# Performance work log

Measured on AMD Instinct MI355X. Metric: run time of the kernel, lower is better.

The kernel has to match this reference:

```python
import jax, jax.numpy as jnp
import numpy as np
import math

EMBED = 256
HEADS = 8
HD = EMBED // HEADS  # 32
NB = 3               # n_behaviors
C = NB * NB + 1      # 10 behavior-pair classes
NUM_BUCKETS = 32
MAX_DIST = 40
EPS = 1e-12
B, L = 4, 512


def _rel_bucket(seq_len, num_buckets=NUM_BUCKETS, max_distance=MAX_DIST):
    """T5-style relative position buckets, matching RelativePositionBias._relative_position_bucket."""
    pos = jnp.arange(seq_len)
    relative_position = pos[None, :] - pos[:, None]  # k - q
    n = -relative_position
    nb = num_buckets // 2
    ret = (n < 0).astype(jnp.int32) * nb
    n = jnp.abs(n)
    max_exact = nb // 2
    is_small = n < max_exact
    nf = jnp.maximum(n, 1).astype(jnp.float32)  # clamp to avoid log(0); masked by is_small anyway
    val_large = max_exact + (jnp.log(nf / max_exact) / math.log(max_distance / max_exact) * (nb - max_exact)).astype(jnp.int32)
    val_large = jnp.minimum(val_large, nb - 1)
    return ret + jnp.where(is_small, n, val_large)


def setup_inputs() -> dict:
    key = jax.random.key(0)
    ks = jax.random.split(key, 12)
    s = 0.02
    return {
        "input_tensor": jax.random.normal(ks[0], (B, L, EMBED), jnp.float32),
        "attention_mask": jnp.zeros((B, 1, L, L), jnp.float32),
        "type_seq": jax.random.randint(ks[1], (B, L), 0, NB + 1),
        "Wq": jax.random.normal(ks[2], (NB + 1, EMBED, HEADS, HD), jnp.float32) * s,
        "Wk": jax.random.normal(ks[3], (NB + 1, EMBED, HEADS, HD), jnp.float32) * s,
        "Wv": jax.random.normal(ks[4], (NB + 1, EMBED, HEADS, HD), jnp.float32) * s,
        "W1": jax.random.normal(ks[5], (NB, HEADS, HD, HD), jnp.float32) * s,
        "alpha1": jax.random.normal(ks[6], (C, NB, HEADS), jnp.float32),
        "W2": jax.random.normal(ks[7], (NB, HEADS, HD, HD), jnp.float32) * s,
        "alpha2": jax.random.normal(ks[8], (C, NB, HEADS), jnp.float32),
        "rp_tables": jax.random.normal(ks[9], (C, NUM_BUCKETS, HEADS), jnp.float32) * s,
        "ln_gamma": jnp.ones((EMBED,), jnp.float32),
        "ln_beta": jnp.zeros((EMBED,), jnp.float32),
    }


def reference(input_tensor, attention_mask, type_seq, Wq, Wk, Wv, W1, alpha1, W2, alpha2, rp_tables, ln_gamma, ln_beta):
    bsz, seq_len, emb = input_tensor.shape
    ts = type_seq
    # behavior pair matrix: 0 if either side is padding, else (tq-1)*NB + tk in [1, NB^2]
    bm = ((ts[:, :, None] * ts[:, None, :]) != 0).astype(jnp.int32)
    bm = bm * ((ts[:, :, None] - 1) * NB + ts[:, None, :])  # [B,L,L]

    # --- relative position bias, gathered per behavior pair ---
    bucket = _rel_bucket(seq_len)                 # [L,L]
    vals = rp_tables[:, bucket, :]                # [C,L,L,H]
    qi = jnp.arange(seq_len)[None, :, None]
    ki = jnp.arange(seq_len)[None, None, :]
    bias = vals[bm, qi, ki]                       # [B,L,L,H] gathered along C per pair
    bias = jnp.transpose(bias, (0, 3, 1, 2))      # [B,H,L,L]

    # --- behavior-gated QKV ---
    oh = jax.nn.one_hot(ts, NB + 1, dtype=input_tensor.dtype)  # [B,L,NB+1]
    q = jnp.einsum('BLH,bHhd,BLb->BhLd', input_tensor, Wq, oh)
    k = jnp.einsum('BLH,bHhd,BLb->BhLd', input_tensor, Wk, oh)
    v = jnp.einsum('BLH,bHhd,BLb->BhLd', input_tensor, Wv, oh)

    # --- bilinear scores with per-pair mixing matrices ---
    W1_ = jnp.einsum('bhmn,Cbh->Chmn', W1, jax.nn.softmax(alpha1, axis=1))
    att_all = jnp.einsum('BhQm,Chmn,BhKn->BhQKC', q, W1_, k)  # [B,H,L,L,C]
    scores = jnp.take_along_axis(att_all, bm[:, None, :, :, None], axis=4)[..., 0]
    scores = scores * (1.0 / math.sqrt(HD)) + bias + attention_mask
    probs = jax.nn.softmax(scores, axis=-1)  # dropout=0.0 -> identity

    # --- behavior-mixed value aggregation ---
    W2_ = jnp.einsum('bhmn,Cbh->Chmn', W2, jax.nn.softmax(alpha2, axis=1))
    oh_bm = jax.nn.one_hot(bm, C, dtype=probs.dtype)          # [B,L,L,C]
    pC = probs[:, :, :, :, None] * oh_bm[:, None]             # [B,H,L,L,C]
    ctx = jnp.einsum('BhQKC,Chnm,BhKn->BhQm', pC, W2_, v)     # [B,H,L,d]

    ctx = jnp.transpose(ctx, (0, 2, 1, 3)).reshape(bsz, seq_len, emb)
    x = ctx + input_tensor  # out_dropout=0.0
    mu = jnp.mean(x, axis=-1, keepdims=True)
    var = jnp.mean(jnp.square(x - mu), axis=-1, keepdims=True)
    return (x - mu) / jnp.sqrt(var + EPS) * ln_gamma + ln_beta
```

## Files before the change

kernel.cpp:

```cpp
#include <hip/hip_runtime.h>
#include <math.h>

#define BB 4
#define LL 512
#define EMB 256
#define NH 8
#define HD 32
#define NB_ 3
#define CCN 10
#define NBKT 32
#define SCALE 0.17677669529663687f

typedef __bf16 bf16_t;
typedef __attribute__((ext_vector_type(8))) bf16_t bf16x8;
typedef __attribute__((ext_vector_type(4))) float f32x4;

__device__ __forceinline__ unsigned short f2b(float f) {
    unsigned int u = __float_as_uint(f);
    u += 0x7FFF + ((u >> 16) & 1);
    return (unsigned short)(u >> 16);
}
__device__ __forceinline__ float b2f(unsigned short s) {
    return __uint_as_float(((unsigned int)s) << 16);
}
__device__ __forceinline__ unsigned pack2(float a, float b) {
    return (unsigned)f2b(a) | ((unsigned)f2b(b) << 16);
}
__device__ __forceinline__ int bm_of(int tq, int tk) {
    return (tq * tk != 0) ? ((tq - 1) * 3 + tk) : 0;
}
__device__ __forceinline__ unsigned long long shfl_up64(unsigned long long v, int d) {
    unsigned lo = (unsigned)__shfl_up((int)(unsigned)v, d, 64);
    unsigned hi = (unsigned)__shfl_up((int)(v >> 32), d, 64);
    return (((unsigned long long)hi) << 32) | lo;
}

__device__ __forceinline__ void sort512(const int* __restrict__ tsb, int* spk,
                                        unsigned long long* wtll, int* msc, int tid) {
    int ty0 = tsb[2 * tid], ty1 = tsb[2 * tid + 1];
    unsigned long long pk = (1ULL << (16 * ty0)) + (1ULL << (16 * ty1));
    unsigned long long v = pk;
    int lane = tid & 63;
#pragma unroll
    for (int off = 1; off < 64; off <<= 1) {
        unsigned long long o = shfl_up64(v, off);
        if (lane >= off) v += o;
    }
    int w = tid >> 6;
    if (lane == 63) wtll[w] = v;
    __syncthreads();
    unsigned long long pre = 0, tot = 0;
#pragma unroll
    for (int i = 0; i < 4; i++) {
        unsigned long long xx = wtll[i];
        if (i < w) pre += xx;
        tot += xx;
    }
    v += pre;
    unsigned long long excl = v - pk;
    int c0 = (int)(tot & 0xFFFF), c1 = (int)((tot >> 16) & 0xFFFF);
    int c2 = (int)((tot >> 32) & 0xFFFF), c3 = (int)((tot >> 48) & 0xFFFF);
    int ub0 = 0, ub1 = c0, ub2 = c0 + c1, ub3 = c0 + c1 + c2;
    if (tid == 0) {
        int pc0 = (c0 + 31) & ~31, pc1 = (c1 + 31) & ~31, pc2 = (c2 + 31) & ~31, pc3 = (c3 + 31) & ~31;
        int pb1 = pc0, pb2 = pc0 + pc1, pb3 = pc0 + pc1 + pc2;
        msc[0] = 0;  msc[1] = pb1; msc[2] = pb2; msc[3] = pb3;
        msc[4] = ub0; msc[5] = ub1; msc[6] = ub2; msc[7] = ub3;
        msc[8] = c0; msc[9] = c1; msc[10] = c2; msc[11] = c3;
        msc[12] = (pb3 + pc3 + 63) & ~63;
    }
    int bases[4] = {ub0, ub1, ub2, ub3};
    int r0 = (int)((excl >> (16 * ty0)) & 0xFFFF);
    unsigned long long excl1 = excl + (1ULL << (16 * ty0));
    int r1 = (int)((excl1 >> (16 * ty1)) & 0xFFFF);
    spk[bases[ty0] + r0] = (ty0 << 16) | (2 * tid);
    spk[bases[ty1] + r1] = (ty1 << 16) | (2 * tid + 1);
    __syncthreads();
}

__device__ __forceinline__ void pad_lookup(const int* msc, int pos, int& real, int& upos, int& seg) {
    seg = (pos >= msc[1]) + (pos >= msc[2]) + (pos >= msc[3]);
    int r = pos - msc[seg];
    real = (r < msc[8 + seg]) ? 1 : 0;
    upos = msc[4 + seg] + r;
}

__global__ void k_pre(const float* __restrict__ A1, const float* __restrict__ W1,
                      const float* __restrict__ A2, const float* __restrict__ W2,
                      const float* __restrict__ Wq, const float* __restrict__ Wk, const float* __restrict__ Wv,
                      const float* __restrict__ am, const int* __restrict__ ts,
                      float* __restrict__ W1s, float* __restrict__ W2s,
                      unsigned short* __restrict__ W1Tb, unsigned short* __restrict__ W2Tb,
                      unsigned short* __restrict__ Wt, int* __restrict__ mflagArr,
                      int* __restrict__ spkg, int* __restrict__ mscg, int* __restrict__ kpadg,
                      short* __restrict__ tblg) {
    __shared__ float cmb[32 * 33];
    __shared__ unsigned short ls[64 * 264];
    __shared__ int reds[4];
    __shared__ int spk_s[LL];
    __shared__ unsigned long long wtll[4];
    __shared__ int msc_s[16];
    int g = blockIdx.x, tid = threadIdx.x;
    if (g < 160) {
        int idx = g;
        const float* alpha = (idx < 80) ? A1 : A2;
        const float* W     = (idx < 80) ? W1 : W2;
        float* Ws          = (idx < 80) ? W1s : W2s;
        unsigned short* WT = (idx < 80) ? W1Tb : W2Tb;
        idx %= 80;
        int cc = idx / NH, h = idx % NH;
        float a0 = alpha[cc * NB_ * NH + 0 * NH + h];
        float a1 = alpha[cc * NB_ * NH + 1 * NH + h];
        float a2 = alpha[cc * NB_ * NH + 2 * NH + h];
        float mx = fmaxf(a0, fmaxf(a1, a2));
        float e0 = __expf(a0 - mx), e1 = __expf(a1 - mx), e2 = __expf(a2 - mx);
        float inv = 1.0f / (e0 + e1 + e2);
        e0 *= inv; e1 *= inv; e2 *= inv;
        for (int i = tid; i < HD * HD; i += 256) {
            int m = i >> 5, n = i & 31;
            float acc = e0 * W[((0 * NH + h) * HD + m) * HD + n]
                      + e1 * W[((1 * NH + h) * HD + m) * HD + n]
                      + e2 * W[((2 * NH + h) * HD + m) * HD + n];
            cmb[m * 33 + n] = acc;
        }
        __syncthreads();
        for (int i = tid; i < HD * HD; i += 256) {
            int a = i >> 5, bq = i & 31;
            Ws[((cc * NH + h) * HD + a) * HD + bq] = cmb[a * 33 + bq];
            WT[((size_t)(cc * NH + h) * HD + a) * HD + bq] = f2b(cmb[bq * 33 + a]);
        }
        return;
    }
    if (g < 208) {
        int t = g - 160;
        int tw = t >> 2, ob = t & 3;
        int which = tw >> 2, ty = tw & 3;
        const float* src = ((which == 0) ? Wq : (which == 1) ? Wk : Wv) + (size_t)ty * EMB * EMB;
        int out0 = ob * 64;
        for (int it = 0; it < 16; it++) {
            int e = it * 16 + (tid >> 4);
            int o4 = (tid & 15) * 4;
            float4 v = *(const float4*)&src[(size_t)e * EMB + out0 + o4];
            ls[(o4 + 0) * 264 + e] = f2b(v.x);
            ls[(o4 + 1) * 264 + e] = f2b(v.y);
            ls[(o4 + 2) * 264 + e] = f2b(v.z);
            ls[(o4 + 3) * 264 + e] = f2b(v.w);
        }
        __syncthreads();
        int out = tid >> 2, ech = (tid & 3) * 8;
        unsigned short* dst = Wt + (size_t)tw * EMB * EMB + (size_t)(out0 + out) * EMB;
        const unsigned short* srcl = &ls[out * 264];
#pragma unroll
        for (int jj = 0; jj < 8; jj++)
            *(uint4*)&dst[ech + jj * 32] = *(const uint4*)&srcl[ech + jj * 32];
        return;
    }
    if (g < 464) {
        int idx = g - 208;
        const uint4* p = (const uint4*)am + (size_t)idx * 1024;
        unsigned o = 0;
#pragma unroll
        for (int j = 0; j < 4; j++) {
            uint4 v = p[tid + j * 256];
            o |= v.x | v.y | v.z | v.w;
        }
        int wv = __any(o != 0);
        if ((tid & 63) == 0) reds[tid >> 6] = wv;
        __syncthreads();
        if (tid == 0) mflagArr[idx] = reds[0] | reds[1] | reds[2] | reds[3];
        return;
    }
    if (g < 468) {
        int b = g - 464;
        sort512(ts + b * LL, spk_s, wtll, msc_s, tid);
        for (int i = tid; i < LL; i += 256) spkg[b * LL + i] = spk_s[i];
        if (tid < 16) mscg[b * 16 + tid] = msc_s[tid];
        int KT = msc_s[12];
        for (int pos = tid; pos < KT; pos += 256) {
            int real, upos, seg;
            pad_lookup(msc_s, pos, real, upos, seg);
            int orig = real ? (spk_s[upos] & 0xFFFF) : 0x3FF;
            kpadg[b * 640 + pos] = (seg << 20) | ((real ? upos : 0) << 10) | orig;
        }
        return;
    }
    for (int d = tid; d < LL; d += 256) {
        int v;
        if (d < 8) v = d;
        else {
            double r = log((double)d / 8.0) / log(5.0);
            v = 8 + (int)(r * 8.0);
            if (v > 15) v = 15;
        }
        tblg[d] = (short)v;
    }
}

__global__ __launch_bounds__(256, 4) void k_qkv(
    const float* __restrict__ x, const int* __restrict__ spkg, const int* __restrict__ mscg,
    const unsigned short* __restrict__ Wt,
    unsigned short* __restrict__ qp, unsigned short* __restrict__ kp,
    unsigned short* __restrict__ vpT) {
    __shared__ int spk[LL];
    __shared__ int msc[16];
    __shared__ unsigned short vt_l[128 * 33];

    int g = blockIdx.x, tid = threadIdx.x;
    int ns = g % 6, gb = g / 6;
    int b = gb >> 4, tb = gb & 15, i0 = tb * 32;
    int which = ns >> 1, nh = ns & 1;
    int wave = tid >> 6, lane = tid & 63, quad = lane >> 4, col = lane & 15;

    spk[tid] = spkg[b * LL + tid];
    spk[tid + 256] = spkg[b * LL + tid + 256];
    if (tid < 16) msc[tid] = mscg[b * 16 + tid];
    __syncthreads();

    bf16x8 afr[2][8];
#pragma unroll
    for (int mt = 0; mt < 2; mt++) {
        int orig = spk[i0 + mt * 16 + col] & 0xFFFF;
        const float* xr = &x[(size_t)(b * LL + orig) * EMB];
#pragma unroll
        for (int kc = 0; kc < 8; kc++) {
            float4 v0 = *(const float4*)&xr[kc * 32 + quad * 8];
            float4 v1 = *(const float4*)&xr[kc * 32 + quad * 8 + 4];
            uint4 up;
            up.x = pack2(v0.x, v0.y); up.y = pack2(v0.z, v0.w);
            up.z = pack2(v1.x, v1.y); up.w = pack2(v1.z, v1.w);
            afr[mt][kc] = *(bf16x8*)&up;
        }
    }
    int t_start = spk[i0] >> 16, t_end = spk[i0 + 31] >> 16;
    unsigned short* outp = (which == 0) ? qp : kp;

    for (int ty = t_start; ty <= t_end; ty++) {
        f32x4 acc[2][2];
#pragma unroll
        for (int mt = 0; mt < 2; mt++)
#pragma unroll
            for (int nt = 0; nt < 2; nt++) acc[mt][nt] = (f32x4){0.f, 0.f, 0.f, 0.f};
        const unsigned short* wsrc = Wt + (size_t)(which * 4 + ty) * EMB * EMB + (size_t)(nh * 128) * EMB;
        const unsigned short* w0 = &wsrc[(size_t)((wave * 2 + 0) * 16 + col) * EMB + quad * 8];
        const unsigned short* w1 = &wsrc[(size_t)((wave * 2 + 1) * 16 + col) * EMB + quad * 8];
#pragma unroll
        for (int kc = 0; kc < 8; kc++) {
            bf16x8 b0 = *(const bf16x8*)&w0[kc * 32];
            bf16x8 b1 = *(const bf16x8*)&w1[kc * 32];
            acc[0][0] = __builtin_amdgcn_mfma_f32_16x16x32_bf16(afr[0][kc], b0, acc[0][0], 0, 0, 0);
            acc[0][1] = __builtin_amdgcn_mfma_f32_16x16x32_bf16(afr[0][kc], b1, acc[0][1], 0, 0, 0);
            acc[1][0] = __builtin_amdgcn_mfma_f32_16x16x32_bf16(afr[1][kc], b0, acc[1][0], 0, 0, 0);
            acc[1][1] = __builtin_amdgcn_mfma_f32_16x16x32_bf16(afr[1][kc], b1, acc[1][1], 0, 0, 0);
        }
        if (which < 2) {
#pragma unroll
            for (int mt = 0; mt < 2; mt++)
#pragma unroll
                for (int r = 0; r < 4; r++) {
                    int tokloc = mt * 16 + quad * 4 + r;
                    int tty = spk[i0 + tokloc] >> 16;
                    if (tty != ty) continue;
#pragma unroll
                    for (int nt = 0; nt < 2; nt++) {
                        int n = nh * 128 + (wave * 2 + nt) * 16 + col;
                        int h = n >> 5, d = n & 31;
                        outp[((size_t)(b * NH + h) * LL + i0 + tokloc) * HD + d] = f2b(acc[mt][nt][r]);
                    }
                }
        } else {
#pragma unroll
            for (int mt = 0; mt < 2; mt++)
#pragma unroll
                for (int nt = 0; nt < 2; nt++) {
                    int ln = (wave * 2 + nt) * 16 + col;
#pragma unroll
                    for (int r = 0; r < 4; r++)
                        vt_l[ln * 33 + mt * 16 + quad * 4 + r] = f2b(acc[mt][nt][r]);
                }
            __syncthreads();
            int ub = msc[4 + ty], cnt = msc[8 + ty], pb = msc[ty];
            int lo = ub - i0; if (lo < 0) lo = 0;
            int hi = ub + cnt - i0; if (hi > 32) hi = 32;
            int run = hi - lo;
            int pbase = pb + i0 + lo - ub;
            int rowbase = b * 256 + nh * 128;
            int t32 = tid & 31;
            if (t32 < run) {
                for (int rr = tid >> 5; rr < 128; rr += 8)
                    vpT[(size_t)(rowbase + rr) * 640 + pbase + t32] = vt_l[rr * 33 + lo + t32];
            }
            __syncthreads();
        }
    }
}

#define SCP 648
#define OFF_UN   20736
#define OFF_QTB  29184
#define OFF_KPAD 33536
#define OFF_TBL  36096
#define OFF_RPL  37120
#define OFF_QOR  38400
#define OFF_QTY  38464
#define OFF_INV  38528
#define SM_TOTAL 38592
__global__ __launch_bounds__(256, 4) void k_attn(
    const unsigned short* __restrict__ qp, const unsigned short* __restrict__ kp,
    const unsigned short* __restrict__ vpT,
    const int* __restrict__ spkg, const int* __restrict__ mscg, const int* __restrict__ kpadg,
    const short* __restrict__ tblg,
    const float* __restrict__ rp, const float* __restrict__ am,
    const float* __restrict__ W1s, const float* __restrict__ W2s,
    const unsigned short* __restrict__ W1Tb, const unsigned short* __restrict__ W2Tb,
    const int* __restrict__ mflagArr, float* __restrict__ ctx) {
    __shared__ __align__(16) char smem[SM_TOTAL];
    __shared__ int msk_s;
    unsigned short* scu = (unsigned short*)smem;
    unsigned short* qstb = (unsigned short*)(smem + OFF_UN);
    float* sb   = (float*)(smem + OFF_UN);
    unsigned short* qtb = (unsigned short*)(smem + OFF_QTB);
    unsigned short* sbb = (unsigned short*)(smem + OFF_QTB);
    int*   kpad = (int*)(smem + OFF_KPAD);
    short* tbl  = (short*)(smem + OFF_TBL);
    float* rp_l = (float*)(smem + OFF_RPL);
    int*   qor_l = (int*)(smem + OFF_QOR);
    int*   qty_l = (int*)(smem + OFF_QTY);
    float* inv_l = (float*)(smem + OFF_INV);

    int blk = blockIdx.x;
    int b = blk >> 8, h = (blk >> 5) & 7, q16 = blk & 31;
    int i0q = q16 * 16;
    int tid = threadIdx.x;
    int wave = tid >> 6, lane = tid & 63, quad = lane >> 4, col = lane & 15;
    int bh = b * NH + h;

    int KT = mscg[b * 16 + 12];
    if (wave == 0) {
        int v = 0;
#pragma unroll
        for (int j = 0; j < 4; j++) v |= mflagArr[lane + 64 * j];
        int anyv = __any(v != 0);
        if (lane == 0) msk_s = anyv;
    }
    if (tid < 16) {
        int v = spkg[b * LL + i0q + tid];
        qor_l[tid] = v & 0xFFFF; qty_l[tid] = v >> 16;
    }
    for (int pos = tid; pos < KT; pos += 256) kpad[pos] = kpadg[b * 640 + pos];
    ((int*)tbl)[tid] = ((const int*)tblg)[tid];
    for (int i = tid; i < CCN * NBKT; i += 256) rp_l[i] = rp[i * NH + h];
    {
        int q = tid >> 4, m2 = (tid & 15) * 2;
        ((unsigned*)qstb)[q * 20 + (tid & 15)] =
            *(const unsigned*)&qp[((size_t)bh * LL + i0q + q) * HD + m2];
    }
    __syncthreads();

    int qor_r[4], qty_r[4];
#pragma unroll
    for (int r = 0; r < 4; r++) { qor_r[r] = qor_l[quad * 4 + r]; qty_r[r] = qty_l[quad * 4 + r]; }
    bool uniq = (qty_l[0] == qty_l[15]);
    int tqu = qty_l[0];
    int tA = qty_l[0], tB = qty_l[15];
    bool two = false;
    if (!uniq) {
        two = true;
#pragma unroll
        for (int i = 0; i < 16; i++) {
            int t = qty_l[i];
            two = two && (t == tA || t == tB);
        }
    }
    int mz = (msk_s == 0);

    if (uniq) {
#pragma unroll
        for (int it = 0; it < 2; it++) {
            int t8 = wave * 2 + it;
            int tk = t8 >> 1, nhf = t8 & 1;
            int bmv = bm_of(tqu, tk);
            bf16x8 a = *(const bf16x8*)&qstb[col * 40 + quad * 8];
            bf16x8 bb = *(const bf16x8*)&W1Tb[((size_t)(bmv * NH + h) * HD + nhf * 16 + col) * HD + quad * 8];
            f32x4 d = {0.f, 0.f, 0.f, 0.f};
            d = __builtin_amdgcn_mfma_f32_16x16x32_bf16(a, bb, d, 0, 0, 0);
#pragma unroll
            for (int r = 0; r < 4; r++)
                qtb[(quad * 4 + r) * 136 + tk * 32 + nhf * 16 + col] = f2b(d[r]);
        }
    } else if (two) {
#pragma unroll
        for (int it = 0; it < 2; it++) {
            int t8 = wave * 2 + it;
            int tk = t8 >> 1, nhf = t8 & 1;
            bf16x8 a = *(const bf16x8*)&qstb[col * 40 + quad * 8];
            bf16x8 bA = *(const bf16x8*)&W1Tb[((size_t)(bm_of(tA, tk) * NH + h) * HD + nhf * 16 + col) * HD + quad * 8];
            bf16x8 bBv = *(const bf16x8*)&W1Tb[((size_t)(bm_of(tB, tk) * NH + h) * HD + nhf * 16 + col) * HD + quad * 8];
            f32x4 dA = {0.f, 0.f, 0.f, 0.f};
            f32x4 dB = {0.f, 0.f, 0.f, 0.f};
            dA = __builtin_amdgcn_mfma_f32_16x16x32_bf16(a, bA, dA, 0, 0, 0);
            dB = __builtin_amdgcn_mfma_f32_16x16x32_bf16(a, bBv, dB, 0, 0, 0);
#pragma unroll
            for (int r = 0; r < 4; r++) {
                float val = (qty_r[r] == tA) ? dA[r] : dB[r];
                qtb[(quad * 4 + r) * 136 + tk * 32 + nhf * 16 + col] = f2b(val);
            }
        }
    } else {
        for (int i = tid; i < 16 * 128; i += 256) {
            int q = i >> 7, r = i & 127, tk = r >> 5, n = r & 31;
            int bmv = bm_of(qty_l[q], tk);
            const float* wb = &W1s[((bmv * NH + h) * HD) * HD + n];
            float acc = 0.f;
#pragma unroll
            for (int m = 0; m < HD; m++) acc += b2f(qstb[q * 40 + m]) * wb[m * HD];
            qtb[q * 136 + tk * 32 + n] = f2b(acc);
        }
    }
    __syncthreads();

    const float* amb = am + (size_t)b * LL * LL;
    int ntiles = KT >> 4;
    for (int tile = wave; tile < ntiles; tile += 4) {
        int kb = tile * 16;
        int kv0 = kpad[kb];
        if ((kv0 & 0x3FF) == 0x3FF) {
#pragma unroll
            for (int r = 0; r < 4; r++) scu[(quad * 4 + r) * SCP + kb + col] = 0xFF80;
            continue;
        }
        int tkt = kv0 >> 20;
        int kpi = kb + col;
        int kv = kpad[kpi];
        int ko = kv & 0x3FF;
        int upos = (kv >> 10) & 0x3FF;
        bool real = (ko != 0x3FF);
        bf16x8 bfr;
        if (real) bfr = *(const bf16x8*)&kp[((size_t)bh * LL + upos) * HD + quad * 8];
        else { uint4 z = make_uint4(0, 0, 0, 0); bfr = *(bf16x8*)&z; }
        bf16x8 a = *(const bf16x8*)&qtb[col * 136 + tkt * 32 + quad * 8];
        f32x4 d = {0.f, 0.f, 0.f, 0.f};
        d = __builtin_amdgcn_mfma_f32_16x16x32_bf16(a, bfr, d, 0, 0, 0);
        if (!real) {
#pragma unroll
            for (int r = 0; r < 4; r++) scu[(quad * 4 + r) * SCP + kpi] = 0xFF80;
        } else {
#pragma unroll
            for (int r = 0; r < 4; r++) {
                int q = quad * 4 + r;
                int qo = qor_r[r];
                int dd = qo - ko;
                int ad = dd < 0 ? -dd : dd;
                int bk = (dd < 0 ? 16 : 0) + (int)tbl[ad];
                float sv = d[r] * SCALE + rp_l[bm_of(qty_r[r], tkt) * NBKT + bk];
                if (!mz) sv += amb[(size_t)qo * LL + ko];
                scu[q * SCP + kpi] = f2b(sv);
            }
        }
    }
    __syncthreads();

    {
        int gq = tid >> 4, t16 = tid & 15;
        float mx = -1e30f;
        for (int kk = t16; kk < KT; kk += 16) mx = fmaxf(mx, b2f(scu[gq * SCP + kk]));
#pragma unroll
        for (int off = 1; off < 16; off <<= 1) mx = fmaxf(mx, __shfl_xor(mx, off, 16));
        float sum = 0.f;
        for (int kk = t16; kk < KT; kk += 16) {
            int idx = gq * SCP + kk;
            float e = __expf(b2f(scu[idx]) - mx);
            scu[idx] = f2b(e); sum += e;
        }
#pragma unroll
        for (int off = 1; off < 16; off <<= 1) sum += __shfl_xor(sum, off, 16);
        if (t16 == 0) inv_l[gq] = 1.0f / sum;
    }
    __syncthreads();

    const unsigned short* vbase = &vpT[(size_t)(b * 256 + h * 32) * 640];
    f32x4 accv[2];
    accv[0] = (f32x4){0.f, 0.f, 0.f, 0.f};
    accv[1] = (f32x4){0.f, 0.f, 0.f, 0.f};
    {
        int pb = mscg[b * 16 + wave];
        int cnt = mscg[b * 16 + 8 + wave];
        int g0 = pb >> 5, g1 = (pb + cnt + 31) >> 5;
        for (int gg = g0; gg < g1; ++gg) {
            int loc = gg << 5;
            bf16x8 a = *(const bf16x8*)&scu[col * SCP + loc + quad * 8];
            bf16x8 b0 = *(const bf16x8*)&vbase[(size_t)col * 640 + loc + quad * 8];
            bf16x8 b1 = *(const bf16x8*)&vbase[(size_t)(col + 16) * 640 + loc + quad * 8];
            accv[0] = __builtin_amdgcn_mfma_f32_16x16x32_bf16(a, b0, accv[0], 0, 0, 0);
            accv[1] = __builtin_amdgcn_mfma_f32_16x16x32_bf16(a, b1, accv[1], 0, 0, 0);
        }
    }
#pragma unroll
    for (int hh = 0; hh < 2; hh++)
#pragma unroll
        for (int r = 0; r < 4; r++) {
            int q = quad * 4 + r, n = col + 16 * hh;
            float fin = accv[hh][r];
            sb[q * 132 + wave * 32 + n] = fin;
            sbb[q * 136 + wave * 32 + n] = f2b(fin);
        }
    __syncthreads();

    if (uniq) {
        if (wave < 2) {
            int mhf = wave;
            f32x4 d = {0.f, 0.f, 0.f, 0.f};
#pragma unroll
            for (int tk = 0; tk < 4; tk++) {
                int bmv = bm_of(tqu, tk);
                bf16x8 a = *(const bf16x8*)&sbb[col * 136 + tk * 32 + quad * 8];
                bf16x8 bb = *(const bf16x8*)&W2Tb[((size_t)(bmv * NH + h) * HD + mhf * 16 + col) * HD + quad * 8];
                d = __builtin_amdgcn_mfma_f32_16x16x32_bf16(a, bb, d, 0, 0, 0);
            }
#pragma unroll
            for (int r = 0; r < 4; r++) {
                int q = quad * 4 + r;
                ctx[((size_t)(b * LL + qor_l[q])) * EMB + h * HD + mhf * 16 + col] = d[r] * inv_l[q];
            }
        }
    } else if (two) {
        int myT = (wave < 2) ? tA : tB;
        int mhf = wave & 1;
        f32x4 d = {0.f, 0.f, 0.f, 0.f};
#pragma unroll
        for (int tk = 0; tk < 4; tk++) {
            int bmv = bm_of(myT, tk);
            bf16x8 a = *(const bf16x8*)&sbb[col * 136 + tk * 32 + quad * 8];
            bf16x8 bb = *(const bf16x8*)&W2Tb[((size_t)(bmv * NH + h) * HD + mhf * 16 + col) * HD + quad * 8];
            d = __builtin_amdgcn_mfma_f32_16x16x32_bf16(a, bb, d, 0, 0, 0);
        }
#pragma unroll
        for (int r = 0; r < 4; r++) {
            int q = quad * 4 + r;
            if (qty_l[q] == myT)
                ctx[((size_t)(b * LL + qor_l[q])) * EMB + h * HD + mhf * 16 + col] = d[r] * inv_l[q];
        }
    } else {
        int m = tid & 31, qq = tid >> 5;
#pragma unroll
        for (int rep = 0; rep < 2; rep++) {
            int qi = qq + 8 * rep;
            int tq = qty_l[qi];
            float acc = 0.f;
#pragma unroll
            for (int tk2 = 0; tk2 < 4; tk2++) {
                int bmv = bm_of(tq, tk2);
                const float* wb = &W2s[((bmv * NH + h) * HD) * HD + m];
                const float* sbp = &sb[qi * 132 + tk2 * 32];
                for (int n = 0; n < HD; n++) acc += sbp[n] * wb[n * HD];
            }
            int qo = qor_l[qi];
            ctx[((size_t)(b * LL + qo)) * EMB + h * HD + m] = acc * inv_l[qi];
        }
    }
}

__global__ void k_ln(const float* __restrict__ ctx, const float* __restrict__ x,
                     const float* __restrict__ gamma, const float* __restrict__ beta,
                     float* __restrict__ out) {
    int wave = threadIdx.x >> 6, lane = threadIdx.x & 63;
    int tok = blockIdx.x * 4 + wave;
    size_t base = (size_t)tok * EMB + lane * 4;
    float4 c = *(const float4*)&ctx[base];
    float4 xi = *(const float4*)&x[base];
    float4 v;
    v.x = c.x + xi.x; v.y = c.y + xi.y; v.z = c.z + xi.z; v.w = c.w + xi.w;
    float s = v.x + v.y + v.z + v.w;
    float s2 = v.x * v.x + v.y * v.y + v.z * v.z + v.w * v.w;
#pragma unroll
    for (int off = 1; off < 64; off <<= 1) {
        s += __shfl_xor(s, off, 64);
        s2 += __shfl_xor(s2, off, 64);
    }
    float mu = s * (1.0f / EMB);
    float var = s2 * (1.0f / EMB) - mu * mu;
    float r = rsqrtf(var + 1e-12f);
    float4 gg = *(const float4*)&gamma[lane * 4];
    float4 bb = *(const float4*)&beta[lane * 4];
    float4 o;
    o.x = (v.x - mu) * r * gg.x + bb.x;
    o.y = (v.y - mu) * r * gg.y + bb.y;
    o.z = (v.z - mu) * r * gg.z + bb.z;
    o.w = (v.w - mu) * r * gg.w + bb.w;
    *(float4*)&out[base] = o;
}

extern "C" void kernel_launch(void* const* d_in, const int* in_sizes, int n_in,
                              void* d_out, int out_size, void* d_ws, size_t ws_size,
                              hipStream_t stream) {
    const float* x  = (const float*)d_in[0];
    const float* am = (const float*)d_in[1];
    const int*   ts = (const int*)d_in[2];
    const float* Wq = (const float*)d_in[3];
    const float* Wk = (const float*)d_in[4];
    const float* Wv = (const float*)d_in[5];
    const float* W1 = (const float*)d_in[6];
    const float* a1 = (const float*)d_in[7];
    const float* W2 = (const float*)d_in[8];
    const float* a2 = (const float*)d_in[9];
    const float* rp = (const float*)d_in[10];
    const float* g  = (const float*)d_in[11];
    const float* be = (const float*)d_in[12];
    float* out = (float*)d_out;

    float* ws  = (float*)d_ws;
    float* W1s = ws;
    float* W2s = ws + 81920;
    unsigned short* W1Tb = (unsigned short*)(ws + 163840);
    unsigned short* W2Tb = (unsigned short*)(ws + 204800);
    int* mflagArr = (int*)(ws + 245760);
    int* spkg = (int*)(ws + 246016);
    int* mscg = (int*)(ws + 248064);
    int* kpadg = (int*)(ws + 248128);
    short* tblg = (short*)(ws + 250688);
    unsigned short* qp = (unsigned short*)(ws + 250944);
    unsigned short* kp = qp + BB * NH * LL * HD;
    unsigned short* vpT = kp + BB * NH * LL * HD;
    float* ctx = (float*)(vpT + BB * 256 * 640);
    unsigned short* Wt = (unsigned short*)ctx;

    hipLaunchKernelGGL(k_pre, dim3(469), dim3(256), 0, stream,
                       a1, W1, a2, W2, Wq, Wk, Wv, am, ts, W1s, W2s, W1Tb, W2Tb, Wt,
                       mflagArr, spkg, mscg, kpadg, tblg);
    hipLaunchKernelGGL(k_qkv, dim3(384), dim3(256), 0, stream, x, spkg, mscg, Wt, qp, kp, vpT);
    hipLaunchKernelGGL(k_attn, dim3(BB * NH * 32), dim3(256), 0, stream,
                       qp, kp, vpT, spkg, mscg, kpadg, tblg, rp, am, W1s, W2s, W1Tb, W2Tb, mflagArr, ctx);
    hipLaunchKernelGGL(k_ln, dim3(BB * LL / 4), dim3(256), 0, stream, ctx, x, g, be, out);
}
```

Baseline: 127.5 us.

## Fuse LayerNorm into attention via completion counters and rebalance prep work across kernels

The W1/W2 mixing precompute and the attention-mask nonzero scan move from the prep kernel into extra blocks of the QKV kernel, so the prep kernel shrinks to 53 blocks and those jobs run alongside the projection. The separate LayerNorm kernel is removed. The last of the 8 head blocks for each query tile, found with an atomic counter, applies residual-add plus LayerNorm to that tile's rows. The mask flag becomes a single atomicOr word, and the kpad copy is vectorised. This removes one launch and the round trip of the ctx tensor, but adds a threadfence and atomic per block and depends on counters being reset in the prep kernel every call.

```diff
diff --git a/kernel.cpp b/kernel.cpp
--- a/kernel.cpp
+++ b/kernel.cpp
@@ -85,54 +85,17 @@
     upos = msc[4 + seg] + r;
 }
 
-__global__ void k_pre(const float* __restrict__ A1, const float* __restrict__ W1,
-                      const float* __restrict__ A2, const float* __restrict__ W2,
-                      const float* __restrict__ Wq, const float* __restrict__ Wk, const float* __restrict__ Wv,
-                      const float* __restrict__ am, const int* __restrict__ ts,
-                      float* __restrict__ W1s, float* __restrict__ W2s,
-                      unsigned short* __restrict__ W1Tb, unsigned short* __restrict__ W2Tb,
-                      unsigned short* __restrict__ Wt, int* __restrict__ mflagArr,
+__global__ void k_pre(const float* __restrict__ Wq, const float* __restrict__ Wk, const float* __restrict__ Wv,
+                      const int* __restrict__ ts, unsigned short* __restrict__ Wt,
                       int* __restrict__ spkg, int* __restrict__ mscg, int* __restrict__ kpadg,
-                      short* __restrict__ tblg) {
-    __shared__ float cmb[32 * 33];
+                      short* __restrict__ tblg, int* __restrict__ cntg) {
     __shared__ unsigned short ls[64 * 264];
-    __shared__ int reds[4];
     __shared__ int spk_s[LL];
     __shared__ unsigned long long wtll[4];
     __shared__ int msc_s[16];
     int g = blockIdx.x, tid = threadIdx.x;
-    if (g < 160) {
-        int idx = g;
-        const float* alpha = (idx < 80) ? A1 : A2;
-        const float* W     = (idx < 80) ? W1 : W2;
-        float* Ws          = (idx < 80) ? W1s : W2s;
-        unsigned short* WT = (idx < 80) ? W1Tb : W2Tb;
-        idx %= 80;
-        int cc = idx / NH, h = idx % NH;
-        float a0 = alpha[cc * NB_ * NH + 0 * NH + h];
-        float a1 = alpha[cc * NB_ * NH + 1 * NH + h];
-        float a2 = alpha[cc * NB_ * NH + 2 * NH + h];
-        float mx = fmaxf(a0, fmaxf(a1, a2));
-        float e0 = __expf(a0 - mx), e1 = __expf(a1 - mx), e2 = __expf(a2 - mx);
-        float inv = 1.0f / (e0 + e1 + e2);
-        e0 *= inv; e1 *= inv; e2 *= inv;
-        for (int i = tid; i < HD * HD; i += 256) {
-            int m = i >> 5, n = i & 31;
-            float acc = e0 * W[((0 * NH + h) * HD + m) * HD + n]
-                      + e1 * W[((1 * NH + h) * HD + m) * HD + n]
-                      + e2 * W[((2 * NH + h) * HD + m) * HD + n];
-            cmb[m * 33 + n] = acc;
-        }
-        __syncthreads();
-        for (int i = tid; i < HD * HD; i += 256) {
-            int a = i >> 5, bq = i & 31;
-            Ws[((cc * NH + h) * HD + a) * HD + bq] = cmb[a * 33 + bq];
-            WT[((size_t)(cc * NH + h) * HD + a) * HD + bq] = f2b(cmb[bq * 33 + a]);
-        }
-        return;
-    }
-    if (g < 208) {
-        int t = g - 160;
+    if (g < 48) {
+        int t = g;
         int tw = t >> 2, ob = t & 3;
         int which = tw >> 2, ty = tw & 3;
         const float* src = ((which == 0) ? Wq : (which == 1) ? Wk : Wv) + (size_t)ty * EMB * EMB;
@@ -155,23 +118,22 @@
             *(uint4*)&dst[ech + jj * 32] = *(const uint4*)&srcl[ech + jj * 32];
         return;
     }
-    if (g < 464) {
-        int idx = g - 208;
-        const uint4* p = (const uint4*)am + (size_t)idx * 1024;
-        unsigned o = 0;
-#pragma unroll
-        for (int j = 0; j < 4; j++) {
-            uint4 v = p[tid + j * 256];
-            o |= v.x | v.y | v.z | v.w;
-        }
-        int wv = __any(o != 0);
-        if ((tid & 63) == 0) reds[tid >> 6] = wv;
-        __syncthreads();
-        if (tid == 0) mflagArr[idx] = reds[0] | reds[1] | reds[2] | reds[3];
+    if (g == 48) {
+        for (int d = tid; d < LL; d += 256) {
+            int v;
+            if (d < 8) v = d;
+            else {
+                double r = log((double)d / 8.0) / log(5.0);
+                v = 8 + (int)(r * 8.0);
+                if (v > 15) v = 15;
+            }
+            tblg[d] = (short)v;
+        }
+        if (tid < 129) cntg[tid] = 0;
         return;
     }
-    if (g < 468) {
-        int b = g - 464;
+    {
+        int b = g - 49;
         sort512(ts + b * LL, spk_s, wtll, msc_s, tid);
         for (int i = tid; i < LL; i += 256) spkg[b * LL + i] = spk_s[i];
         if (tid < 16) mscg[b * 16 + tid] = msc_s[tid];
@@ -182,30 +144,72 @@
             int orig = real ? (spk_s[upos] & 0xFFFF) : 0x3FF;
             kpadg[b * 640 + pos] = (seg << 20) | ((real ? upos : 0) << 10) | orig;
         }
-        return;
-    }
-    for (int d = tid; d < LL; d += 256) {
-        int v;
-        if (d < 8) v = d;
-        else {
-            double r = log((double)d / 8.0) / log(5.0);
-            v = 8 + (int)(r * 8.0);
-            if (v > 15) v = 15;
-        }
-        tblg[d] = (short)v;
     }
 }
 
 __global__ __launch_bounds__(256, 4) void k_qkv(
     const float* __restrict__ x, const int* __restrict__ spkg, const int* __restrict__ mscg,
     const unsigned short* __restrict__ Wt,
+    const float* __restrict__ A1, const float* __restrict__ W1,
+    const float* __restrict__ A2, const float* __restrict__ W2,
+    const float* __restrict__ am,
+    float* __restrict__ W1s, float* __restrict__ W2s,
+    unsigned short* __restrict__ W1Tb, unsigned short* __restrict__ W2Tb,
+    int* __restrict__ cntg,
     unsigned short* __restrict__ qp, unsigned short* __restrict__ kp,
     unsigned short* __restrict__ vpT) {
     __shared__ int spk[LL];
     __shared__ int msc[16];
-    __shared__ unsigned short vt_l[128 * 33];
+    __shared__ __align__(16) unsigned short vt_l[128 * 33];
 
     int g = blockIdx.x, tid = threadIdx.x;
+
+    if (g >= 384) {
+        int gg = g - 384;
+        if (gg < 160) {
+            float* cmbf = (float*)vt_l;
+            int idx = gg;
+            const float* alpha = (idx < 80) ? A1 : A2;
+            const float* W     = (idx < 80) ? W1 : W2;
+            float* Ws          = (idx < 80) ? W1s : W2s;
+            unsigned short* WT = (idx < 80) ? W1Tb : W2Tb;
+            idx %= 80;
+            int cc = idx / NH, h = idx % NH;
+            float a0 = alpha[cc * NB_ * NH + 0 * NH + h];
+            float a1 = alpha[cc * NB_ * NH + 1 * NH + h];
+            float a2 = alpha[cc * NB_ * NH + 2 * NH + h];
+            float mx = fmaxf(a0, fmaxf(a1, a2));
+            float e0 = __expf(a0 - mx), e1 = __expf(a1 - mx), e2 = __expf(a2 - mx);
+            float inv = 1.0f / (e0 + e1 + e2);
+            e0 *= inv; e1 *= inv; e2 *= inv;
+            for (int i = tid; i < HD * HD; i += 256) {
+                int m = i >> 5, n = i & 31;
+                float acc = e0 * W[((0 * NH + h) * HD + m) * HD + n]
+                          + e1 * W[((1 * NH + h) * HD + m) * HD + n]
+                          + e2 * W[((2 * NH + h) * HD + m) * HD + n];
+                cmbf[m * 33 + n] = acc;
+            }
+            __syncthreads();
+            for (int i = tid; i < HD * HD; i += 256) {
+                int a = i >> 5, bq = i & 31;
+                Ws[((cc * NH + h) * HD + a) * HD + bq] = cmbf[a * 33 + bq];
+                WT[((size_t)(cc * NH + h) * HD + a) * HD + bq] = f2b(cmbf[bq * 33 + a]);
+            }
+        } else {
+            int idx = gg - 160;
+            const uint4* p = (const uint4*)am + (size_t)idx * 1024;
+            unsigned o = 0;
+#pragma unroll
+            for (int j = 0; j < 4; j++) {
+                uint4 v = p[tid + j * 256];
+                o |= v.x | v.y | v.z | v.w;
+            }
+            int wv = __any(o != 0);
+            if ((tid & 63) == 0 && wv) atomicOr(&cntg[128], 1);
+        }
+        return;
+    }
+
     int ns = g % 6, gb = g / 6;
     int b = gb >> 4, tb = gb & 15, i0 = tb * 32;
     int which = ns >> 1, nh = ns & 1;
@@ -312,9 +316,12 @@
     const float* __restrict__ rp, const float* __restrict__ am,
     const float* __restrict__ W1s, const float* __restrict__ W2s,
     const unsigned short* __restrict__ W1Tb, const unsigned short* __restrict__ W2Tb,
-    const int* __restrict__ mflagArr, float* __restrict__ ctx) {
+    int* __restrict__ cntg, float* __restrict__ ctx,
+    const float* __restrict__ x, const float* __restrict__ gamma, const float* __restrict__ beta,
+    float* __restrict__ out) {
     __shared__ __align__(16) char smem[SM_TOTAL];
     __shared__ int msk_s;
+    __shared__ int done_s;
     unsigned short* scu = (unsigned short*)smem;
     unsigned short* qstb = (unsigned short*)(smem + OFF_UN);
     float* sb   = (float*)(smem + OFF_UN);
@@ -335,18 +342,12 @@
     int bh = b * NH + h;
 
     int KT = mscg[b * 16 + 12];
-    if (wave == 0) {
-        int v = 0;
-#pragma unroll
-        for (int j = 0; j < 4; j++) v |= mflagArr[lane + 64 * j];
-        int anyv = __any(v != 0);
-        if (lane == 0) msk_s = anyv;
-    }
+    if (tid == 0) msk_s = cntg[128];
     if (tid < 16) {
         int v = spkg[b * LL + i0q + tid];
         qor_l[tid] = v & 0xFFFF; qty_l[tid] = v >> 16;
     }
-    for (int pos = tid; pos < KT; pos += 256) kpad[pos] = kpadg[b * 640 + pos];
+    if (tid < (KT >> 2)) ((int4*)kpad)[tid] = ((const int4*)(kpadg + b * 640))[tid];
     ((int*)tbl)[tid] = ((const int*)tblg)[tid];
     for (int i = tid; i < CCN * NBKT; i += 256) rp_l[i] = rp[i * NH + h];
     {
@@ -557,36 +558,65 @@
             ctx[((size_t)(b * LL + qo)) * EMB + h * HD + m] = acc * inv_l[qi];
         }
     }
-}
-
-__global__ void k_ln(const float* __restrict__ ctx, const float* __restrict__ x,
-                     const float* __restrict__ gamma, const float* __restrict__ beta,
-                     float* __restrict__ out) {
-    int wave = threadIdx.x >> 6, lane = threadIdx.x & 63;
-    int tok = blockIdx.x * 4 + wave;
-    size_t base = (size_t)tok * EMB + lane * 4;
-    float4 c = *(const float4*)&ctx[base];
-    float4 xi = *(const float4*)&x[base];
-    float4 v;
-    v.x = c.x + xi.x; v.y = c.y + xi.y; v.z = c.z + xi.z; v.w = c.w + xi.w;
-    float s = v.x + v.y + v.z + v.w;
-    float s2 = v.x * v.x + v.y * v.y + v.z * v.z + v.w * v.w;
-#pragma unroll
-    for (int off = 1; off < 64; off <<= 1) {
-        s += __shfl_xor(s, off, 64);
-        s2 += __shfl_xor(s2, off, 64);
-    }
-    float mu = s * (1.0f / EMB);
-    float var = s2 * (1.0f / EMB) - mu * mu;
-    float r = rsqrtf(var + 1e-12f);
-    float4 gg = *(const float4*)&gamma[lane * 4];
-    float4 bb = *(const float4*)&beta[lane * 4];
-    float4 o;
-    o.x = (v.x - mu) * r * gg.x + bb.x;
-    o.y = (v.y - mu) * r * gg.y + bb.y;
-    o.z = (v.z - mu) * r * gg.z + bb.z;
-    o.w = (v.w - mu) * r * gg.w + bb.w;
-    *(float4*)&out[base] = o;
+
+    __threadfence();
+    __syncthreads();
+    if (tid == 0) done_s = atomicAdd(&cntg[b * 32 + q16], 1);
+    __syncthreads();
+    if (done_s == 7) {
+        __threadfence();
+        int qi = tid >> 4, t16 = tid & 15;
+        int tok = qor_l[qi];
+        size_t base = ((size_t)(b * LL + tok)) * EMB + t16 * 16;
+        float4 c0 = *(const float4*)&ctx[base + 0];
+        float4 c1 = *(const float4*)&ctx[base + 4];
+        float4 c2 = *(const float4*)&ctx[base + 8];
+        float4 c3 = *(const float4*)&ctx[base + 12];
+        float4 x0 = *(const float4*)&x[base + 0];
+        float4 x1 = *(const float4*)&x[base + 4];
+        float4 x2 = *(const float4*)&x[base + 8];
+        float4 x3 = *(const float4*)&x[base + 12];
+        c0.x += x0.x; c0.y += x0.y; c0.z += x0.z; c0.w += x0.w;
+        c1.x += x1.x; c1.y += x1.y; c1.z += x1.z; c1.w += x1.w;
+        c2.x += x2.x; c2.y += x2.y; c2.z += x2.z; c2.w += x2.w;
+        c3.x += x3.x; c3.y += x3.y; c3.z += x3.z; c3.w += x3.w;
+        float s = c0.x + c0.y + c0.z + c0.w + c1.x + c1.y + c1.z + c1.w
+                + c2.x + c2.y + c2.z + c2.w + c3.x + c3.y + c3.z + c3.w;
+        float s2 = c0.x*c0.x + c0.y*c0.y + c0.z*c0.z + c0.w*c0.w
+                 + c1.x*c1.x + c1.y*c1.y + c1.z*c1.z + c1.w*c1.w
+                 + c2.x*c2.x + c2.y*c2.y + c2.z*c2.z + c2.w*c2.w
+                 + c3.x*c3.x + c3.y*c3.y + c3.z*c3.z + c3.w*c3.w;
+#pragma unroll
+        for (int off = 1; off < 16; off <<= 1) {
+            s += __shfl_xor(s, off, 16);
+            s2 += __shfl_xor(s2, off, 16);
+        }
+        float mu = s * (1.0f / EMB);
+        float var = s2 * (1.0f / EMB) - mu * mu;
+        float rr = rsqrtf(var + 1e-12f);
+        int go = t16 * 16;
+        float4 g0 = *(const float4*)&gamma[go + 0];
+        float4 g1 = *(const float4*)&gamma[go + 4];
+        float4 g2 = *(const float4*)&gamma[go + 8];
+        float4 g3 = *(const float4*)&gamma[go + 12];
+        float4 b0 = *(const float4*)&beta[go + 0];
+        float4 b1 = *(const float4*)&beta[go + 4];
+        float4 b2 = *(const float4*)&beta[go + 8];
+        float4 b3 = *(const float4*)&beta[go + 12];
+        float4 o0, o1, o2, o3;
+        o0.x = (c0.x - mu) * rr * g0.x + b0.x; o0.y = (c0.y - mu) * rr * g0.y + b0.y;
+        o0.z = (c0.z - mu) * rr * g0.z + b0.z; o0.w = (c0.w - mu) * rr * g0.w + b0.w;
+        o1.x = (c1.x - mu) * rr * g1.x + b1.x; o1.y = (c1.y - mu) * rr * g1.y + b1.y;
+        o1.z = (c1.z - mu) * rr * g1.z + b1.z; o1.w = (c1.w - mu) * rr * g1.w + b1.w;
+        o2.x = (c2.x - mu) * rr * g2.x + b2.x; o2.y = (c2.y - mu) * rr * g2.y + b2.y;
+        o2.z = (c2.z - mu) * rr * g2.z + b2.z; o2.w = (c2.w - mu) * rr * g2.w + b2.w;
+        o3.x = (c3.x - mu) * rr * g3.x + b3.x; o3.y = (c3.y - mu) * rr * g3.y + b3.y;
+        o3.z = (c3.z - mu) * rr * g3.z + b3.z; o3.w = (c3.w - mu) * rr * g3.w + b3.w;
+        *(float4*)&out[base + 0] = o0;
+        *(float4*)&out[base + 4] = o1;
+        *(float4*)&out[base + 8] = o2;
+        *(float4*)&out[base + 12] = o3;
+    }
 }
 
 extern "C" void kernel_launch(void* const* d_in, const int* in_sizes, int n_in,
@@ -612,7 +642,7 @@
     float* W2s = ws + 81920;
     unsigned short* W1Tb = (unsigned short*)(ws + 163840);
     unsigned short* W2Tb = (unsigned short*)(ws + 204800);
-    int* mflagArr = (int*)(ws + 245760);
+    int* cntg = (int*)(ws + 245760);
     int* spkg = (int*)(ws + 246016);
     int* mscg = (int*)(ws + 248064);
     int* kpadg = (int*)(ws + 248128);
@@ -623,11 +653,12 @@
     float* ctx = (float*)(vpT + BB * 256 * 640);
     unsigned short* Wt = (unsigned short*)ctx;
 
-    hipLaunchKernelGGL(k_pre, dim3(469), dim3(256), 0, stream,
-                       a1, W1, a2, W2, Wq, Wk, Wv, am, ts, W1s, W2s, W1Tb, W2Tb, Wt,
-                       mflagArr, spkg, mscg, kpadg, tblg);
-    hipLaunchKernelGGL(k_qkv, dim3(384), dim3(256), 0, stream, x, spkg, mscg, Wt, qp, kp, vpT);
+    hipLaunchKernelGGL(k_pre, dim3(53), dim3(256), 0, stream,
+                       Wq, Wk, Wv, ts, Wt, spkg, mscg, kpadg, tblg, cntg);
+    hipLaunchKernelGGL(k_qkv, dim3(800), dim3(256), 0, stream,
+                       x, spkg, mscg, Wt, a1, W1, a2, W2, am, W1s, W2s, W1Tb, W2Tb, cntg,
+                       qp, kp, vpT);
     hipLaunchKernelGGL(k_attn, dim3(BB * NH * 32), dim3(256), 0, stream,
-                       qp, kp, vpT, spkg, mscg, kpadg, tblg, rp, am, W1s, W2s, W1Tb, W2Tb, mflagArr, ctx);
-    hipLaunchKernelGGL(k_ln, dim3(BB * LL / 4), dim3(256), 0, stream, ctx, x, g, be, out);
-}
+                       qp, kp, vpT, spkg, mscg, kpadg, tblg, rp, am, W1s, W2s, W1Tb, W2Tb,
+                       cntg, ctx, x, g, be, out);
+}
```

Result: slower. 252.1 us (+97.7%).

## Move W1/W2 mixing and mask scan into QKV kernel as extra blocks

Applied to the files above, without the earlier changes.

The mixing-matrix softmax/combination and the attention-mask nonzero scan move out of the pre kernel into extra blocks of the QKV projection kernel, so they run alongside the projection. The pre kernel shrinks to weight transpose, sorting and the bucket table. The per-block mask flag array becomes a single atomically-ORed flag that the pre kernel zeroes, which removes the 256-entry reduction in every attention block. The kpad staging load is vectorised to int4. The aim is to shorten the critical path of the small pre kernel. The risks are that the QKV kernel now has more blocks competing for compute units, and that the int4 copy assumes KT is a multiple of 4.

```diff
diff --git a/kernel.cpp b/kernel.cpp
--- a/kernel.cpp
+++ b/kernel.cpp
@@ -85,54 +85,17 @@
     upos = msc[4 + seg] + r;
 }
 
-__global__ void k_pre(const float* __restrict__ A1, const float* __restrict__ W1,
-                      const float* __restrict__ A2, const float* __restrict__ W2,
-                      const float* __restrict__ Wq, const float* __restrict__ Wk, const float* __restrict__ Wv,
-                      const float* __restrict__ am, const int* __restrict__ ts,
-                      float* __restrict__ W1s, float* __restrict__ W2s,
-                      unsigned short* __restrict__ W1Tb, unsigned short* __restrict__ W2Tb,
-                      unsigned short* __restrict__ Wt, int* __restrict__ mflagArr,
+__global__ void k_pre(const float* __restrict__ Wq, const float* __restrict__ Wk, const float* __restrict__ Wv,
+                      const int* __restrict__ ts, unsigned short* __restrict__ Wt,
                       int* __restrict__ spkg, int* __restrict__ mscg, int* __restrict__ kpadg,
-                      short* __restrict__ tblg) {
-    __shared__ float cmb[32 * 33];
+                      short* __restrict__ tblg, int* __restrict__ cntg) {
     __shared__ unsigned short ls[64 * 264];
-    __shared__ int reds[4];
     __shared__ int spk_s[LL];
     __shared__ unsigned long long wtll[4];
     __shared__ int msc_s[16];
     int g = blockIdx.x, tid = threadIdx.x;
-    if (g < 160) {
-        int idx = g;
-        const float* alpha = (idx < 80) ? A1 : A2;
-        const float* W     = (idx < 80) ? W1 : W2;
-        float* Ws          = (idx < 80) ? W1s : W2s;
-        unsigned short* WT = (idx < 80) ? W1Tb : W2Tb;
-        idx %= 80;
-        int cc = idx / NH, h = idx % NH;
-        float a0 = alpha[cc * NB_ * NH + 0 * NH + h];
-        float a1 = alpha[cc * NB_ * NH + 1 * NH + h];
-        float a2 = alpha[cc * NB_ * NH + 2 * NH + h];
-        float mx = fmaxf(a0, fmaxf(a1, a2));
-        float e0 = __expf(a0 - mx), e1 = __expf(a1 - mx), e2 = __expf(a2 - mx);
-        float inv = 1.0f / (e0 + e1 + e2);
-        e0 *= inv; e1 *= inv; e2 *= inv;
-        for (int i = tid; i < HD * HD; i += 256) {
-            int m = i >> 5, n = i & 31;
-            float acc = e0 * W[((0 * NH + h) * HD + m) * HD + n]
-                      + e1 * W[((1 * NH + h) * HD + m) * HD + n]
-                      + e2 * W[((2 * NH + h) * HD + m) * HD + n];
-            cmb[m * 33 + n] = acc;
-        }
-        __syncthreads();
-        for (int i = tid; i < HD * HD; i += 256) {
-            int a = i >> 5, bq = i & 31;
-            Ws[((cc * NH + h) * HD + a) * HD + bq] = cmb[a * 33 + bq];
-            WT[((size_t)(cc * NH + h) * HD + a) * HD + bq] = f2b(cmb[bq * 33 + a]);
-        }
-        return;
-    }
-    if (g < 208) {
-        int t = g - 160;
+    if (g < 48) {
+        int t = g;
         int tw = t >> 2, ob = t & 3;
         int which = tw >> 2, ty = tw & 3;
         const float* src = ((which == 0) ? Wq : (which == 1) ? Wk : Wv) + (size_t)ty * EMB * EMB;
@@ -155,23 +118,22 @@
             *(uint4*)&dst[ech + jj * 32] = *(const uint4*)&srcl[ech + jj * 32];
         return;
     }
-    if (g < 464) {
-        int idx = g - 208;
-        const uint4* p = (const uint4*)am + (size_t)idx * 1024;
-        unsigned o = 0;
-#pragma unroll
-        for (int j = 0; j < 4; j++) {
-            uint4 v = p[tid + j * 256];
-            o |= v.x | v.y | v.z | v.w;
-        }
-        int wv = __any(o != 0);
-        if ((tid & 63) == 0) reds[tid >> 6] = wv;
-        __syncthreads();
-        if (tid == 0) mflagArr[idx] = reds[0] | reds[1] | reds[2] | reds[3];
+    if (g == 48) {
+        for (int d = tid; d < LL; d += 256) {
+            int v;
+            if (d < 8) v = d;
+            else {
+                double r = log((double)d / 8.0) / log(5.0);
+                v = 8 + (int)(r * 8.0);
+                if (v > 15) v = 15;
+            }
+            tblg[d] = (short)v;
+        }
+        if (tid == 0) cntg[128] = 0;
         return;
     }
-    if (g < 468) {
-        int b = g - 464;
+    {
+        int b = g - 49;
         sort512(ts + b * LL, spk_s, wtll, msc_s, tid);
         for (int i = tid; i < LL; i += 256) spkg[b * LL + i] = spk_s[i];
         if (tid < 16) mscg[b * 16 + tid] = msc_s[tid];
@@ -182,30 +144,72 @@
             int orig = real ? (spk_s[upos] & 0xFFFF) : 0x3FF;
             kpadg[b * 640 + pos] = (seg << 20) | ((real ? upos : 0) << 10) | orig;
         }
-        return;
-    }
-    for (int d = tid; d < LL; d += 256) {
-        int v;
-        if (d < 8) v = d;
-        else {
-            double r = log((double)d / 8.0) / log(5.0);
-            v = 8 + (int)(r * 8.0);
-            if (v > 15) v = 15;
-        }
-        tblg[d] = (short)v;
     }
 }
 
 __global__ __launch_bounds__(256, 4) void k_qkv(
     const float* __restrict__ x, const int* __restrict__ spkg, const int* __restrict__ mscg,
     const unsigned short* __restrict__ Wt,
+    const float* __restrict__ A1, const float* __restrict__ W1,
+    const float* __restrict__ A2, const float* __restrict__ W2,
+    const float* __restrict__ am,
+    float* __restrict__ W1s, float* __restrict__ W2s,
+    unsigned short* __restrict__ W1Tb, unsigned short* __restrict__ W2Tb,
+    int* __restrict__ cntg,
     unsigned short* __restrict__ qp, unsigned short* __restrict__ kp,
     unsigned short* __restrict__ vpT) {
     __shared__ int spk[LL];
     __shared__ int msc[16];
-    __shared__ unsigned short vt_l[128 * 33];
+    __shared__ __align__(16) unsigned short vt_l[128 * 33];
 
     int g = blockIdx.x, tid = threadIdx.x;
+
+    if (g >= 384) {
+        int gg = g - 384;
+        if (gg < 160) {
+            float* cmbf = (float*)vt_l;
+            int idx = gg;
+            const float* alpha = (idx < 80) ? A1 : A2;
+            const float* W     = (idx < 80) ? W1 : W2;
+            float* Ws          = (idx < 80) ? W1s : W2s;
+            unsigned short* WT = (idx < 80) ? W1Tb : W2Tb;
+            idx %= 80;
+            int cc = idx / NH, h = idx % NH;
+            float a0 = alpha[cc * NB_ * NH + 0 * NH + h];
+            float a1 = alpha[cc * NB_ * NH + 1 * NH + h];
+            float a2 = alpha[cc * NB_ * NH + 2 * NH + h];
+            float mx = fmaxf(a0, fmaxf(a1, a2));
+            float e0 = __expf(a0 - mx), e1 = __expf(a1 - mx), e2 = __expf(a2 - mx);
+            float inv = 1.0f / (e0 + e1 + e2);
+            e0 *= inv; e1 *= inv; e2 *= inv;
+            for (int i = tid; i < HD * HD; i += 256) {
+                int m = i >> 5, n = i & 31;
+                float acc = e0 * W[((0 * NH + h) * HD + m) * HD + n]
+                          + e1 * W[((1 * NH + h) * HD + m) * HD + n]
+                          + e2 * W[((2 * NH + h) * HD + m) * HD + n];
+                cmbf[m * 33 + n] = acc;
+            }
+            __syncthreads();
+            for (int i = tid; i < HD * HD; i += 256) {
+                int a = i >> 5, bq = i & 31;
+                Ws[((cc * NH + h) * HD + a) * HD + bq] = cmbf[a * 33 + bq];
+                WT[((size_t)(cc * NH + h) * HD + a) * HD + bq] = f2b(cmbf[bq * 33 + a]);
+            }
+        } else {
+            int idx = gg - 160;
+            const uint4* p = (const uint4*)am + (size_t)idx * 1024;
+            unsigned o = 0;
+#pragma unroll
+            for (int j = 0; j < 4; j++) {
+                uint4 v = p[tid + j * 256];
+                o |= v.x | v.y | v.z | v.w;
+            }
+            int wv = __any(o != 0);
+            if ((tid & 63) == 0 && wv) atomicOr(&cntg[128], 1);
+        }
+        return;
+    }
+
     int ns = g % 6, gb = g / 6;
     int b = gb >> 4, tb = gb & 15, i0 = tb * 32;
     int which = ns >> 1, nh = ns & 1;
@@ -312,7 +316,7 @@
     const float* __restrict__ rp, const float* __restrict__ am,
     const float* __restrict__ W1s, const float* __restrict__ W2s,
     const unsigned short* __restrict__ W1Tb, const unsigned short* __restrict__ W2Tb,
-    const int* __restrict__ mflagArr, float* __restrict__ ctx) {
+    const int* __restrict__ cntg, float* __restrict__ ctx) {
     __shared__ __align__(16) char smem[SM_TOTAL];
     __shared__ int msk_s;
     unsigned short* scu = (unsigned short*)smem;
@@ -335,18 +339,12 @@
     int bh = b * NH + h;
 
     int KT = mscg[b * 16 + 12];
-    if (wave == 0) {
-        int v = 0;
-#pragma unroll
-        for (int j = 0; j < 4; j++) v |= mflagArr[lane + 64 * j];
-        int anyv = __any(v != 0);
-        if (lane == 0) msk_s = anyv;
-    }
+    if (tid == 0) msk_s = cntg[128];
     if (tid < 16) {
         int v = spkg[b * LL + i0q + tid];
         qor_l[tid] = v & 0xFFFF; qty_l[tid] = v >> 16;
     }
-    for (int pos = tid; pos < KT; pos += 256) kpad[pos] = kpadg[b * 640 + pos];
+    if (tid < (KT >> 2)) ((int4*)kpad)[tid] = ((const int4*)(kpadg + b * 640))[tid];
     ((int*)tbl)[tid] = ((const int*)tblg)[tid];
     for (int i = tid; i < CCN * NBKT; i += 256) rp_l[i] = rp[i * NH + h];
     {
@@ -612,7 +610,7 @@
     float* W2s = ws + 81920;
     unsigned short* W1Tb = (unsigned short*)(ws + 163840);
     unsigned short* W2Tb = (unsigned short*)(ws + 204800);
-    int* mflagArr = (int*)(ws + 245760);
+    int* cntg = (int*)(ws + 245760);
     int* spkg = (int*)(ws + 246016);
     int* mscg = (int*)(ws + 248064);
     int* kpadg = (int*)(ws + 248128);
@@ -623,11 +621,13 @@
     float* ctx = (float*)(vpT + BB * 256 * 640);
     unsigned short* Wt = (unsigned short*)ctx;
 
-    hipLaunchKernelGGL(k_pre, dim3(469), dim3(256), 0, stream,
-                       a1, W1, a2, W2, Wq, Wk, Wv, am, ts, W1s, W2s, W1Tb, W2Tb, Wt,
-                       mflagArr, spkg, mscg, kpadg, tblg);
-    hipLaunchKernelGGL(k_qkv, dim3(384), dim3(256), 0, stream, x, spkg, mscg, Wt, qp, kp, vpT);
+    hipLaunchKernelGGL(k_pre, dim3(53), dim3(256), 0, stream,
+                       Wq, Wk, Wv, ts, Wt, spkg, mscg, kpadg, tblg, cntg);
+    hipLaunchKernelGGL(k_qkv, dim3(800), dim3(256), 0, stream,
+                       x, spkg, mscg, Wt, a1, W1, a2, W2, am, W1s, W2s, W1Tb, W2Tb, cntg,
+                       qp, kp, vpT);
     hipLaunchKernelGGL(k_attn, dim3(BB * NH * 32), dim3(256), 0, stream,
-                       qp, kp, vpT, spkg, mscg, kpadg, tblg, rp, am, W1s, W2s, W1Tb, W2Tb, mflagArr, ctx);
+                       qp, kp, vpT, spkg, mscg, kpadg, tblg, rp, am, W1s, W2s, W1Tb, W2Tb,
+                       cntg, ctx);
     hipLaunchKernelGGL(k_ln, dim3(BB * LL / 4), dim3(256), 0, stream, ctx, x, g, be, out);
 }
```

After: 127.3 us. Within noise of the previous version (-0.2%).
